# Performance work log

Measured on AMD Instinct MI355X. Metric: run time of the kernel, lower is better.

The kernel has to match this reference:

```python
import jax, jax.numpy as jnp
import numpy as np

B, K, D = 32768, 4096, 256


def setup_inputs() -> dict:
    key = jax.random.key(0)
    k1, k2 = jax.random.split(key)
    z_e_x = jax.random.normal(k1, (B, D), dtype=jnp.float32)
    # embedding.weight initialized N(0, 1) per init='normal'
    weight = jax.random.normal(k2, (K, D), dtype=jnp.float32)
    return {"z_e_x": z_e_x, "weight": weight}


def reference(z_e_x, weight):
    # Squared L2 distances ||z - e||^2 = ||z||^2 - 2 z.e + ||e||^2,
    # computed via a GEMM instead of materializing the [B, K, D] broadcast
    # that the torch code builds with repeat(). Same math as
    # sum((z_e_x_ - codebook_vectors)**2, dim=-1).
    z_sq = jnp.sum(z_e_x * z_e_x, axis=-1, keepdims=True)          # [B, 1]
    e_sq = jnp.sum(weight * weight, axis=-1)                        # [K]
    cross = jnp.einsum('bd,kd->bk', z_e_x, weight)                  # [B, K]
    distances = z_sq - 2.0 * cross + e_sq                           # [B, K]
    # greedy=True path of forward()
    index = jnp.argmin(distances, axis=-1)                          # [B] int
    # straight_through(): quantized lookup + straight-through estimator
    z_q_x = weight[index]                                           # [B, D]
    sg_z_e_x = z_e_x + jax.lax.stop_gradient(z_q_x - z_e_x)         # [B, D]
    return (sg_z_e_x, z_q_x, index)
```

## Files before the change

kernel.cpp:

```cpp
#include <hip/hip_runtime.h>

typedef _Float16 half8 __attribute__((ext_vector_type(8)));
typedef _Float16 half4 __attribute__((ext_vector_type(4)));
typedef float floatx16 __attribute__((ext_vector_type(16)));

constexpr int Bn = 32768, Kn = 4096, Dn = 256;
constexpr int BM = 128;
constexpr int NI = 64;
constexpr int NCH = 256;

__global__ void prep_kernel(const float* __restrict__ w, float* __restrict__ esq,
                            char* __restrict__ w16) {
    int code = blockIdx.x * 4 + (threadIdx.x >> 6);
    int l = threadIdx.x & 63;
    float4 v = *reinterpret_cast<const float4*>(w + (size_t)code * Dn + l * 4);
    float s = v.x * v.x + v.y * v.y + v.z * v.z + v.w * v.w;
    #pragma unroll
    for (int off = 32; off; off >>= 1) s += __shfl_xor(s, off);
    if (l == 0) esq[code] = s;

    float fv[4] = {v.x, v.y, v.z, v.w};
    half4 h, lo;
    #pragma unroll
    for (int j = 0; j < 4; ++j) {
        _Float16 hh = (_Float16)fv[j];
        h[j] = hh;
        lo[j] = (_Float16)(fv[j] - (float)hh);
    }
    const int kc = l >> 4;
    const int o_h = (l & 15) * 8;
    const int swz = (code & 15) << 4;
    char* row = w16 + (size_t)code * 1024 + kc * 256;
    *reinterpret_cast<half4*>(row + (o_h ^ swz)) = h;
    *reinterpret_cast<half4*>(row + ((o_h + 128) ^ swz)) = lo;
}

#define GLDS(gsrc, ldsoff)                                                        \
    __builtin_amdgcn_global_load_lds(                                             \
        (const __attribute__((address_space(1))) unsigned int*)(const void*)(gsrc),\
        (__attribute__((address_space(3))) unsigned int*)(void*)(smem + (ldsoff)), \
        16, 0, 0)

#define MFMA(a, b, c) __builtin_amdgcn_mfma_f32_32x32x16_f16((a), (b), (c), 0, 0, 0)

__global__ void
__launch_bounds__(256, 1)
__attribute__((amdgpu_waves_per_eu(1, 1)))
vq_kernel(const float* __restrict__ z, const float* __restrict__ w,
          const float* __restrict__ esq, const char* __restrict__ w16,
          float* __restrict__ out0, float* __restrict__ out1,
          float* __restrict__ out2) {
    __shared__ char smem[84480];
    const int tid = threadIdx.x;
    const int wv = tid >> 6, l = tid & 63;
    const int mw = wv >> 1, nw = wv & 1;
    const int lh = l >> 5, ll = l & 31;
    const int blkRow = blockIdx.x * BM;

    float* esq_s = reinterpret_cast<float*>(smem + 65536);
    #pragma unroll
    for (int j = 0; j < 16; ++j) esq_s[j * 256 + tid] = esq[j * 256 + tid];

    half8 a_hi[32], a_lo[32];
    #pragma unroll
    for (int t = 0; t < 2; ++t) {
        const float* zr = z + (size_t)(blkRow + mw * 64 + t * 32 + ll) * Dn + lh * 8;
        #pragma unroll
        for (int ks = 0; ks < 16; ++ks) {
            float4 f0 = *reinterpret_cast<const float4*>(zr + ks * 16);
            float4 f1 = *reinterpret_cast<const float4*>(zr + ks * 16 + 4);
            float fv[8] = {f0.x, f0.y, f0.z, f0.w, f1.x, f1.y, f1.z, f1.w};
            #pragma unroll
            for (int j = 0; j < 8; ++j) {
                _Float16 h = (_Float16)fv[j];
                a_hi[t * 16 + ks][j] = h;
                a_lo[t * 16 + ks][j] = (_Float16)(fv[j] - (float)h);
            }
        }
    }

    const int G0 = wv * 256 + l;
    const size_t srcOff0 = (size_t)(G0 >> 4) * 1024 + (G0 & 15) * 16;

    int addrH[4], addrL[4];
    {
        const int c_loc = nw * 32 + ll;
        const int swz = (c_loc & 15) << 4;
        #pragma unroll
        for (int ks = 0; ks < 4; ++ks) {
            const int o = ks * 32 + lh * 16;
            addrH[ks] = c_loc * 256 + (o ^ swz);
            addrL[ks] = c_loc * 256 + ((o + 128) ^ swz);
        }
    }

    float rbv0[16], rbv1[16];
    unsigned rbn0[4] = {0, 0, 0, 0}, rbn1[4] = {0, 0, 0, 0};
    #pragma unroll
    for (int q = 0; q < 16; ++q) { rbv0[q] = 3.4e38f; rbv1[q] = 3.4e38f; }

    asm volatile("s_waitcnt vmcnt(0)" ::: "memory");
    __syncthreads();

    {
        const char* s0 = w16 + srcOff0;
        const char* s1 = w16 + 256 + srcOff0;
        const int d0 = wv * 4096, d1 = 16384 + wv * 4096;
        GLDS(s0, d0); GLDS(s0 + 4096, d0 + 1024); GLDS(s0 + 8192, d0 + 2048); GLDS(s0 + 12288, d0 + 3072);
        GLDS(s1, d1); GLDS(s1 + 4096, d1 + 1024); GLDS(s1 + 8192, d1 + 2048); GLDS(s1 + 12288, d1 + 3072);
    }
    asm volatile("s_waitcnt vmcnt(4)" ::: "memory");
    __builtin_amdgcn_s_barrier();
    asm volatile("" ::: "memory");

    half8 sh0[4], sl0[4], sh1[4], sl1[4];
    #pragma unroll
    for (int ks = 0; ks < 4; ++ks) {
        sh0[ks] = *reinterpret_cast<const half8*>(smem + addrH[ks]);
        sl0[ks] = *reinterpret_cast<const half8*>(smem + addrL[ks]);
    }

    for (int ni = 0; ni < NI; ++ni) {
        floatx16 acc0 = {}, acc1 = {};
        #pragma unroll
        for (int kc = 0; kc < 4; ++kc) {
            const int c = ni * 4 + kc;
            if (c + 2 < NCH) {
                const char* s2 = w16 + (size_t)((c + 2) >> 2) * 65536 + ((c + 2) & 3) * 256 + srcOff0;
                const int d2 = (((kc + 2) & 3) * 16384) + wv * 4096;
                GLDS(s2, d2); GLDS(s2 + 4096, d2 + 1024);
                GLDS(s2 + 8192, d2 + 2048); GLDS(s2 + 12288, d2 + 3072);
                asm volatile("s_waitcnt vmcnt(4)" ::: "memory");
            } else {
                asm volatile("s_waitcnt vmcnt(0)" ::: "memory");
            }
            __builtin_amdgcn_s_barrier();
            asm volatile("" ::: "memory");
            const char* nb = smem + ((kc + 1) & 3) * 16384;
            if (kc & 1) {
                if (c + 1 < NCH) {
                    #pragma unroll
                    for (int ks = 0; ks < 4; ++ks) {
                        sh0[ks] = *reinterpret_cast<const half8*>(nb + addrH[ks]);
                        sl0[ks] = *reinterpret_cast<const half8*>(nb + addrL[ks]);
                    }
                }
                __builtin_amdgcn_s_setprio(1);
                #pragma unroll
                for (int ks = 0; ks < 4; ++ks) {
                    const int ksg = kc * 4 + ks;
                    acc0 = MFMA(a_hi[ksg], sh1[ks], acc0);
                    acc1 = MFMA(a_hi[16 + ksg], sh1[ks], acc1);
                    acc0 = MFMA(a_hi[ksg], sl1[ks], acc0);
                    acc1 = MFMA(a_hi[16 + ksg], sl1[ks], acc1);
                    acc0 = MFMA(a_lo[ksg], sh1[ks], acc0);
                    acc1 = MFMA(a_lo[16 + ksg], sh1[ks], acc1);
                }
                __builtin_amdgcn_s_setprio(0);
            } else {
                if (c + 1 < NCH) {
                    #pragma unroll
                    for (int ks = 0; ks < 4; ++ks) {
                        sh1[ks] = *reinterpret_cast<const half8*>(nb + addrH[ks]);
                        sl1[ks] = *reinterpret_cast<const half8*>(nb + addrL[ks]);
                    }
                }
                __builtin_amdgcn_s_setprio(1);
                #pragma unroll
                for (int ks = 0; ks < 4; ++ks) {
                    const int ksg = kc * 4 + ks;
                    acc0 = MFMA(a_hi[ksg], sh0[ks], acc0);
                    acc1 = MFMA(a_hi[16 + ksg], sh0[ks], acc1);
                    acc0 = MFMA(a_hi[ksg], sl0[ks], acc0);
                    acc1 = MFMA(a_hi[16 + ksg], sl0[ks], acc1);
                    acc0 = MFMA(a_lo[ksg], sh0[ks], acc0);
                    acc1 = MFMA(a_lo[16 + ksg], sh0[ks], acc1);
                }
                __builtin_amdgcn_s_setprio(0);
            }
        }
        const float e = esq_s[ni * 64 + nw * 32 + ll];
        #pragma unroll
        for (int q = 0; q < 16; ++q) {
            const int sh = (q & 3) * 8;
            const unsigned msk = ~(255u << sh);
            const float v0 = fmaf(-2.f, acc0[q], e);
            if (v0 < rbv0[q]) { rbv0[q] = v0; rbn0[q >> 2] = (rbn0[q >> 2] & msk) | ((unsigned)ni << sh); }
            const float v1 = fmaf(-2.f, acc1[q], e);
            if (v1 < rbv1[q]) { rbv1[q] = v1; rbn1[q >> 2] = (rbn1[q >> 2] & msk) | ((unsigned)ni << sh); }
        }
    }

    __syncthreads();
    int2* comb = reinterpret_cast<int2*>(smem + 81920);
    #pragma unroll
    for (int q = 0; q < 16; ++q) {
        float v0 = rbv0[q], v1 = rbv1[q];
        int i0 = (int)((rbn0[q >> 2] >> ((q & 3) * 8)) & 255u) * 64 + nw * 32 + ll;
        int i1 = (int)((rbn1[q >> 2] >> ((q & 3) * 8)) & 255u) * 64 + nw * 32 + ll;
        #pragma unroll
        for (int off = 1; off < 32; off <<= 1) {
            float ov0 = __shfl_xor(v0, off); int oi0 = __shfl_xor(i0, off);
            if (ov0 < v0 || (ov0 == v0 && oi0 < i0)) { v0 = ov0; i0 = oi0; }
            float ov1 = __shfl_xor(v1, off); int oi1 = __shfl_xor(i1, off);
            if (ov1 < v1 || (ov1 == v1 && oi1 < i1)) { v1 = ov1; i1 = oi1; }
        }
        if (ll == 0) {
            const int r32 = (q & 3) + 8 * (q >> 2) + 4 * lh;
            comb[(mw * 64 + r32) * 2 + nw] = make_int2(__float_as_int(v0), i0);
            comb[(mw * 64 + 32 + r32) * 2 + nw] = make_int2(__float_as_int(v1), i1);
        }
    }
    __syncthreads();
    int* idxF = reinterpret_cast<int*>(smem + 83968);
    if (tid < 128) {
        int2 c0 = comb[tid * 2], c1 = comb[tid * 2 + 1];
        float v0 = __int_as_float(c0.x), v1 = __int_as_float(c1.x);
        idxF[tid] = (v1 < v0 || (v1 == v0 && c1.y < c0.y)) ? c1.y : c0.y;
    }
    __syncthreads();

    {
        const int r = tid >> 1, p2 = tid & 1;
        const int gRow = blkRow + r;
        const int idx = idxF[r];
        const float* wr = w + (size_t)idx * Dn + p2 * 128;
        const float* zr = z + (size_t)gRow * Dn + p2 * 128;
        float* o0 = out0 + (size_t)gRow * Dn + p2 * 128;
        float* o1 = out1 + (size_t)gRow * Dn + p2 * 128;
        #pragma unroll
        for (int q = 0; q < 32; ++q) {
            float4 wq = *reinterpret_cast<const float4*>(wr + q * 4);
            float4 zq = *reinterpret_cast<const float4*>(zr + q * 4);
            *reinterpret_cast<float4*>(o1 + q * 4) = wq;
            float4 sg;
            sg.x = zq.x + (wq.x - zq.x);
            sg.y = zq.y + (wq.y - zq.y);
            sg.z = zq.z + (wq.z - zq.z);
            sg.w = zq.w + (wq.w - zq.w);
            *reinterpret_cast<float4*>(o0 + q * 4) = sg;
        }
        if (p2 == 0) out2[gRow] = (float)idx;
    }
}

extern "C" void kernel_launch(void* const* d_in, const int* in_sizes, int n_in,
                              void* d_out, int out_size, void* d_ws, size_t ws_size,
                              hipStream_t stream) {
    (void)in_sizes; (void)n_in; (void)out_size; (void)ws_size;
    const float* z = (const float*)d_in[0];
    const float* w = (const float*)d_in[1];
    float* esq = (float*)d_ws;
    char* w16 = (char*)d_ws + 16384;
    float* out0 = (float*)d_out;
    float* out1 = out0 + (size_t)Bn * Dn;
    float* out2 = out1 + (size_t)Bn * Dn;

    prep_kernel<<<Kn / 4, 256, 0, stream>>>(w, esq, w16);
    vq_kernel<<<Bn / BM, 256, 0, stream>>>(z, w, esq, w16, out0, out1, out2);
}
```

Baseline: 318.7 us.

## Double block to 512 threads with 32-row wave tiles and split hi/lo accumulators

The distance kernel moves from 4 waves, each owning 64 rows, to 8 waves, each owning 32 rows. This halves per-wave A-fragment registers, accumulators and per-wave loads of the staged codebook. The hi and lo correction MFMAs now go to a separate accumulator from the hi*hi product, which shortens the dependent accumulator chains. The goal is more waves in flight to hide LDS and MFMA latency. The risk is register pressure: `__launch_bounds__(512, 2)` asks for two resident blocks, but the ~84 KB of shared memory per block may not allow that, and the tighter register cap may cause spills.

```diff
diff --git a/kernel.cpp b/kernel.cpp
--- a/kernel.cpp
+++ b/kernel.cpp
@@ -44,8 +44,7 @@
 #define MFMA(a, b, c) __builtin_amdgcn_mfma_f32_32x32x16_f16((a), (b), (c), 0, 0, 0)
 
 __global__ void
-__launch_bounds__(256, 1)
-__attribute__((amdgpu_waves_per_eu(1, 1)))
+__launch_bounds__(512, 2)
 vq_kernel(const float* __restrict__ z, const float* __restrict__ w,
           const float* __restrict__ esq, const char* __restrict__ w16,
           float* __restrict__ out0, float* __restrict__ out1,
@@ -59,12 +58,11 @@
 
     float* esq_s = reinterpret_cast<float*>(smem + 65536);
     #pragma unroll
-    for (int j = 0; j < 16; ++j) esq_s[j * 256 + tid] = esq[j * 256 + tid];
-
-    half8 a_hi[32], a_lo[32];
-    #pragma unroll
-    for (int t = 0; t < 2; ++t) {
-        const float* zr = z + (size_t)(blkRow + mw * 64 + t * 32 + ll) * Dn + lh * 8;
+    for (int j = 0; j < 8; ++j) esq_s[j * 512 + tid] = esq[j * 512 + tid];
+
+    half8 a_hi[16], a_lo[16];
+    {
+        const float* zr = z + (size_t)(blkRow + mw * 32 + ll) * Dn + lh * 8;
         #pragma unroll
         for (int ks = 0; ks < 16; ++ks) {
             float4 f0 = *reinterpret_cast<const float4*>(zr + ks * 16);
@@ -73,14 +71,14 @@
             #pragma unroll
             for (int j = 0; j < 8; ++j) {
                 _Float16 h = (_Float16)fv[j];
-                a_hi[t * 16 + ks][j] = h;
-                a_lo[t * 16 + ks][j] = (_Float16)(fv[j] - (float)h);
-            }
-        }
-    }
-
-    const int G0 = wv * 256 + l;
-    const size_t srcOff0 = (size_t)(G0 >> 4) * 1024 + (G0 & 15) * 16;
+                a_hi[ks][j] = h;
+                a_lo[ks][j] = (_Float16)(fv[j] - (float)h);
+            }
+        }
+    }
+
+    const size_t srcOff0 = (size_t)(wv * 8 + (l >> 4)) * 1024 + (l & 15) * 16;
+    const int ldsOff0 = wv * 2048;
 
     int addrH[4], addrL[4];
     {
@@ -94,22 +92,19 @@
         }
     }
 
-    float rbv0[16], rbv1[16];
-    unsigned rbn0[4] = {0, 0, 0, 0}, rbn1[4] = {0, 0, 0, 0};
-    #pragma unroll
-    for (int q = 0; q < 16; ++q) { rbv0[q] = 3.4e38f; rbv1[q] = 3.4e38f; }
+    float rbv[16];
+    unsigned rbn[4] = {0, 0, 0, 0};
+    #pragma unroll
+    for (int q = 0; q < 16; ++q) rbv[q] = 3.4e38f;
 
     asm volatile("s_waitcnt vmcnt(0)" ::: "memory");
     __syncthreads();
 
-    {
-        const char* s0 = w16 + srcOff0;
-        const char* s1 = w16 + 256 + srcOff0;
-        const int d0 = wv * 4096, d1 = 16384 + wv * 4096;
-        GLDS(s0, d0); GLDS(s0 + 4096, d0 + 1024); GLDS(s0 + 8192, d0 + 2048); GLDS(s0 + 12288, d0 + 3072);
-        GLDS(s1, d1); GLDS(s1 + 4096, d1 + 1024); GLDS(s1 + 8192, d1 + 2048); GLDS(s1 + 12288, d1 + 3072);
-    }
-    asm volatile("s_waitcnt vmcnt(4)" ::: "memory");
+    GLDS(w16 + srcOff0, ldsOff0);
+    GLDS(w16 + 4096 + srcOff0, ldsOff0 + 1024);
+    GLDS(w16 + 256 + srcOff0, 16384 + ldsOff0);
+    GLDS(w16 + 256 + 4096 + srcOff0, 16384 + ldsOff0 + 1024);
+    asm volatile("s_waitcnt vmcnt(2)" ::: "memory");
     __builtin_amdgcn_s_barrier();
     asm volatile("" ::: "memory");
 
@@ -121,16 +116,16 @@
     }
 
     for (int ni = 0; ni < NI; ++ni) {
-        floatx16 acc0 = {}, acc1 = {};
+        floatx16 accA = {}, accB = {};
         #pragma unroll
         for (int kc = 0; kc < 4; ++kc) {
             const int c = ni * 4 + kc;
             if (c + 2 < NCH) {
                 const char* s2 = w16 + (size_t)((c + 2) >> 2) * 65536 + ((c + 2) & 3) * 256 + srcOff0;
-                const int d2 = (((kc + 2) & 3) * 16384) + wv * 4096;
-                GLDS(s2, d2); GLDS(s2 + 4096, d2 + 1024);
-                GLDS(s2 + 8192, d2 + 2048); GLDS(s2 + 12288, d2 + 3072);
-                asm volatile("s_waitcnt vmcnt(4)" ::: "memory");
+                const int d2 = (((kc + 2) & 3) * 16384) + ldsOff0;
+                GLDS(s2, d2);
+                GLDS(s2 + 4096, d2 + 1024);
+                asm volatile("s_waitcnt vmcnt(2)" ::: "memory");
             } else {
                 asm volatile("s_waitcnt vmcnt(0)" ::: "memory");
             }
@@ -149,12 +144,9 @@
                 #pragma unroll
                 for (int ks = 0; ks < 4; ++ks) {
                     const int ksg = kc * 4 + ks;
-                    acc0 = MFMA(a_hi[ksg], sh1[ks], acc0);
-                    acc1 = MFMA(a_hi[16 + ksg], sh1[ks], acc1);
-                    acc0 = MFMA(a_hi[ksg], sl1[ks], acc0);
-                    acc1 = MFMA(a_hi[16 + ksg], sl1[ks], acc1);
-                    acc0 = MFMA(a_lo[ksg], sh1[ks], acc0);
-                    acc1 = MFMA(a_lo[16 + ksg], sh1[ks], acc1);
+                    accA = MFMA(a_hi[ksg], sh1[ks], accA);
+                    accB = MFMA(a_hi[ksg], sl1[ks], accB);
+                    accB = MFMA(a_lo[ksg], sh1[ks], accB);
                 }
                 __builtin_amdgcn_s_setprio(0);
             } else {
@@ -169,12 +161,9 @@
                 #pragma unroll
                 for (int ks = 0; ks < 4; ++ks) {
                     const int ksg = kc * 4 + ks;
-                    acc0 = MFMA(a_hi[ksg], sh0[ks], acc0);
-                    acc1 = MFMA(a_hi[16 + ksg], sh0[ks], acc1);
-                    acc0 = MFMA(a_hi[ksg], sl0[ks], acc0);
-                    acc1 = MFMA(a_hi[16 + ksg], sl0[ks], acc1);
-                    acc0 = MFMA(a_lo[ksg], sh0[ks], acc0);
-                    acc1 = MFMA(a_lo[16 + ksg], sh0[ks], acc1);
+                    accA = MFMA(a_hi[ksg], sh0[ks], accA);
+                    accB = MFMA(a_hi[ksg], sl0[ks], accB);
+                    accB = MFMA(a_lo[ksg], sh0[ks], accB);
                 }
                 __builtin_amdgcn_s_setprio(0);
             }
@@ -182,33 +171,29 @@
         const float e = esq_s[ni * 64 + nw * 32 + ll];
         #pragma unroll
         for (int q = 0; q < 16; ++q) {
+            const float v = fmaf(-2.f, accA[q], fmaf(-2.f, accB[q], e));
             const int sh = (q & 3) * 8;
-            const unsigned msk = ~(255u << sh);
-            const float v0 = fmaf(-2.f, acc0[q], e);
-            if (v0 < rbv0[q]) { rbv0[q] = v0; rbn0[q >> 2] = (rbn0[q >> 2] & msk) | ((unsigned)ni << sh); }
-            const float v1 = fmaf(-2.f, acc1[q], e);
-            if (v1 < rbv1[q]) { rbv1[q] = v1; rbn1[q >> 2] = (rbn1[q >> 2] & msk) | ((unsigned)ni << sh); }
-        }
-    }
-
-    __syncthreads();
+            if (v < rbv[q]) {
+                rbv[q] = v;
+                rbn[q >> 2] = (rbn[q >> 2] & ~(255u << sh)) | ((unsigned)ni << sh);
+            }
+        }
+    }
+
     int2* comb = reinterpret_cast<int2*>(smem + 81920);
     #pragma unroll
     for (int q = 0; q < 16; ++q) {
-        float v0 = rbv0[q], v1 = rbv1[q];
-        int i0 = (int)((rbn0[q >> 2] >> ((q & 3) * 8)) & 255u) * 64 + nw * 32 + ll;
-        int i1 = (int)((rbn1[q >> 2] >> ((q & 3) * 8)) & 255u) * 64 + nw * 32 + ll;
+        float v = rbv[q];
+        int i = (int)((rbn[q >> 2] >> ((q & 3) * 8)) & 255u) * 64 + nw * 32 + ll;
         #pragma unroll
         for (int off = 1; off < 32; off <<= 1) {
-            float ov0 = __shfl_xor(v0, off); int oi0 = __shfl_xor(i0, off);
-            if (ov0 < v0 || (ov0 == v0 && oi0 < i0)) { v0 = ov0; i0 = oi0; }
-            float ov1 = __shfl_xor(v1, off); int oi1 = __shfl_xor(i1, off);
-            if (ov1 < v1 || (ov1 == v1 && oi1 < i1)) { v1 = ov1; i1 = oi1; }
+            float ov = __shfl_xor(v, off);
+            int oi = __shfl_xor(i, off);
+            if (ov < v || (ov == v && oi < i)) { v = ov; i = oi; }
         }
         if (ll == 0) {
             const int r32 = (q & 3) + 8 * (q >> 2) + 4 * lh;
-            comb[(mw * 64 + r32) * 2 + nw] = make_int2(__float_as_int(v0), i0);
-            comb[(mw * 64 + 32 + r32) * 2 + nw] = make_int2(__float_as_int(v1), i1);
+            comb[(mw * 32 + r32) * 2 + nw] = make_int2(__float_as_int(v), i);
         }
     }
     __syncthreads();
@@ -221,15 +206,15 @@
     __syncthreads();
 
     {
-        const int r = tid >> 1, p2 = tid & 1;
+        const int r = tid >> 2, p4 = tid & 3;
         const int gRow = blkRow + r;
         const int idx = idxF[r];
-        const float* wr = w + (size_t)idx * Dn + p2 * 128;
-        const float* zr = z + (size_t)gRow * Dn + p2 * 128;
-        float* o0 = out0 + (size_t)gRow * Dn + p2 * 128;
-        float* o1 = out1 + (size_t)gRow * Dn + p2 * 128;
-        #pragma unroll
-        for (int q = 0; q < 32; ++q) {
+        const float* wr = w + (size_t)idx * Dn + p4 * 64;
+        const float* zr = z + (size_t)gRow * Dn + p4 * 64;
+        float* o0 = out0 + (size_t)gRow * Dn + p4 * 64;
+        float* o1 = out1 + (size_t)gRow * Dn + p4 * 64;
+        #pragma unroll
+        for (int q = 0; q < 16; ++q) {
             float4 wq = *reinterpret_cast<const float4*>(wr + q * 4);
             float4 zq = *reinterpret_cast<const float4*>(zr + q * 4);
             *reinterpret_cast<float4*>(o1 + q * 4) = wq;
@@ -240,7 +225,7 @@
             sg.w = zq.w + (wq.w - zq.w);
             *reinterpret_cast<float4*>(o0 + q * 4) = sg;
         }
-        if (p2 == 0) out2[gRow] = (float)idx;
+        if (p4 == 0) out2[gRow] = (float)idx;
     }
 }
 
@@ -257,5 +242,5 @@
     float* out2 = out1 + (size_t)Bn * Dn;
 
     prep_kernel<<<Kn / 4, 256, 0, stream>>>(w, esq, w16);
-    vq_kernel<<<Bn / BM, 256, 0, stream>>>(z, w, esq, w16, out0, out1, out2);
+    vq_kernel<<<Bn / BM, 512, 0, stream>>>(z, w, esq, w16, out0, out1, out2);
 }
```

After: 325.6 us. 2.2% more time.
